# Optimization experiments

Measured on AMD Instinct MI355X. Metric: run time of the kernel, lower is better.

## Reference

```python
import jax, jax.numpy as jnp
import numpy as np

B, S, D_IN, D_EMB, H = 2, 2048, 1024, 1024, 16
HD = D_EMB // H

def setup_inputs() -> dict:
    key = jax.random.key(0)
    k1, k2, k3 = jax.random.split(key, 3)
    # xavier-uniform style scales
    lim_qkv = float(np.sqrt(6.0 / (D_IN + 3 * D_EMB)))
    lim_o = float(np.sqrt(6.0 / (D_EMB + D_EMB)))
    return {
        "x": jax.random.normal(k1, (B, S, D_IN), dtype=jnp.float32),
        "W_qkv": jax.random.uniform(k2, (3 * D_EMB, D_IN), minval=-lim_qkv, maxval=lim_qkv, dtype=jnp.float32),
        "b_qkv": jnp.zeros((3 * D_EMB,), dtype=jnp.float32),
        "W_o": jax.random.uniform(k3, (D_EMB, D_EMB), minval=-lim_o, maxval=lim_o, dtype=jnp.float32),
        "b_o": jnp.zeros((D_EMB,), dtype=jnp.float32),
    }

def reference(x, W_qkv, b_qkv, W_o, b_o):
    b, s, _ = x.shape
    qkv = x @ W_qkv.T + b_qkv                     # [B,S,3E]
    qkv = qkv.reshape(b, s, H, 3 * HD).transpose(0, 2, 1, 3)  # [B,H,S,3*HD]
    q, k, v = jnp.split(qkv, 3, axis=-1)          # each [B,H,S,HD]
    scale = 1.0 / np.sqrt(HD)
    attn = jax.nn.softmax(jnp.einsum('bhqd,bhkd->bhqk', q, k) * scale, axis=-1)
    vals = jnp.einsum('bhqk,bhkd->bhqd', attn, v) # [B,H,S,HD]
    vals = vals.transpose(0, 2, 1, 3).reshape(b, s, D_EMB)
    return vals @ W_o.T + b_o
```

## Files before the change

kernel.cpp:

```cpp
#include <hip/hip_runtime.h>
#include <hip/hip_bf16.h>

typedef unsigned short u16;
typedef unsigned int u32;
typedef __bf16 bf16x8 __attribute__((ext_vector_type(8)));
typedef float f32x4 __attribute__((ext_vector_type(4)));
typedef u32 u32x4 __attribute__((ext_vector_type(4)));

#define MFMA16(a, b, c) __builtin_amdgcn_mfma_f32_16x16x32_bf16((a), (b), (c), 0, 0, 0)

static __device__ __forceinline__ u16 f2bf(float f) {
  __hip_bfloat16 h = __float2bfloat16(f);
  return __builtin_bit_cast(u16, h);
}

static __device__ __forceinline__ u32 pack2(float a, float b) {
  return (u32)f2bf(a) | ((u32)f2bf(b) << 16);
}

static __device__ __forceinline__ bf16x8 ldbf8(const void* p) {
  return *reinterpret_cast<const bf16x8*>(p);
}

static __device__ __forceinline__ void gload_lds16(const void* g, void* l) {
  __builtin_amdgcn_global_load_lds(
      (const __attribute__((address_space(1))) u32*)g,
      (__attribute__((address_space(3))) u32*)l, 16, 0, 0);
}

__global__ void cvt_bf16(const float* __restrict__ s, u16* __restrict__ d, int n8) {
  int i = blockIdx.x * 256 + threadIdx.x;
  if (i >= n8) return;
  const float4* p = reinterpret_cast<const float4*>(s) + (size_t)i * 2;
  float4 a = p[0], b = p[1];
  uint4 o;
  o.x = (u32)f2bf(a.x) | ((u32)f2bf(a.y) << 16);
  o.y = (u32)f2bf(a.z) | ((u32)f2bf(a.w) << 16);
  o.z = (u32)f2bf(b.x) | ((u32)f2bf(b.y) << 16);
  o.w = (u32)f2bf(b.z) | ((u32)f2bf(b.w) << 16);
  reinterpret_cast<uint4*>(d)[i] = o;
}

template <bool BF16OUT>
__global__ __launch_bounds__(256, 3) void gemm_bt(const u16* __restrict__ A,
                                                  const u16* __restrict__ Bm,
                                                  const float* __restrict__ bias,
                                                  void* __restrict__ Cp,
                                                  int M, int N, int K) {
  __shared__ __align__(16) char As[128 * 64 * 2];
  __shared__ __align__(16) char Bs[128 * 64 * 2];
  const int tid = threadIdx.x;
  const int lane = tid & 63;
  const int wid = tid >> 6;
  const int fr = lane & 15, fg = lane >> 4;
  const int gx = gridDim.x, nwg = gx * gridDim.y;
  const int id = blockIdx.y * gx + blockIdx.x;
  const int nid = (id & 7) * (nwg >> 3) + (id >> 3);
  const int bm = nid / gx, bn = nid % gx;
  const int wm = (wid >> 1) * 64, wn = (wid & 1) * 64;

  f32x4 acc[4][4];
#pragma unroll
  for (int i = 0; i < 4; ++i)
#pragma unroll
    for (int j = 0; j < 4; ++j) acc[i][j] = (f32x4){0.f, 0.f, 0.f, 0.f};

  const int nk = K >> 6;
  for (int kt = 0; kt < nk; ++kt) {
#pragma unroll
    for (int it = 0; it < 4; ++it) {
      int q = it * 256 + tid;
      int row = q >> 3;
      int c = (q & 7) ^ (row & 7);
      gload_lds16(A + (size_t)(bm * 128 + row) * K + kt * 64 + c * 8, As + q * 16);
      gload_lds16(Bm + (size_t)(bn * 128 + row) * K + kt * 64 + c * 8, Bs + q * 16);
    }
    __syncthreads();
#pragma unroll
    for (int mk = 0; mk < 2; ++mk) {
      bf16x8 af[4], bfr[4];
#pragma unroll
      for (int i = 0; i < 4; ++i) {
        int row = wm + i * 16 + fr;
        af[i] = ldbf8(As + ((row * 128 + mk * 64 + fg * 16) ^ ((row & 7) << 4)));
      }
#pragma unroll
      for (int j = 0; j < 4; ++j) {
        int row = wn + j * 16 + fr;
        bfr[j] = ldbf8(Bs + ((row * 128 + mk * 64 + fg * 16) ^ ((row & 7) << 4)));
      }
#pragma unroll
      for (int i = 0; i < 4; ++i)
#pragma unroll
        for (int j = 0; j < 4; ++j) acc[i][j] = MFMA16(af[i], bfr[j], acc[i][j]);
    }
    __syncthreads();
  }

#pragma unroll
  for (int j = 0; j < 4; ++j) {
    int col = bn * 128 + wn + j * 16 + fr;
    float bv = bias[col];
#pragma unroll
    for (int i = 0; i < 4; ++i) {
#pragma unroll
      for (int r = 0; r < 4; ++r) {
        int row = bm * 128 + wm + i * 16 + fg * 4 + r;
        float v = acc[i][j][r] + bv;
        if (BF16OUT)
          ((u16*)Cp)[(size_t)row * N + col] = f2bf(v);
        else
          ((float*)Cp)[(size_t)row * N + col] = v;
      }
    }
  }
}

__global__ __launch_bounds__(512, 4) void attn_fwd(const u16* __restrict__ qkv,
                                                   u16* __restrict__ aout) {
  const int qt = blockIdx.x;
  const int bh = blockIdx.y;
  const int b = bh >> 4, h = bh & 15;
  const int tid = threadIdx.x, lane = tid & 63, wid = tid >> 6;
  const int fr = lane & 15, fg = (lane >> 4) & 3;

  __shared__ __align__(16) char Ks[2][64 * 128];
  __shared__ __align__(16) char VTs[2][64 * 128];

  const int q0 = qt * 128 + wid * 16;
  const size_t bS = (size_t)b * 2048;
  const u16* kbase = qkv + bS * 3072 + h * 192 + 64;
  const u16* vbase = qkv + bS * 3072 + h * 192 + 128;

  const int krow = tid >> 3;
  const int kcol = (tid & 7) * 8;
  int kwo = (krow * 128 + (tid & 7) * 16) ^ ((krow & 7) << 4);
  asm volatile("" : "+v"(kwo));
  const int vg = (tid >> 4) & 3;
  const int vs2 = 32 * (wid >> 2) + 16 * (vg >> 1) + 4 * (wid & 3) + 2 * (vg & 1);
  const int vdc = (tid & 15) * 4;
  const int vm_ = vs2 >> 5, vG = (vs2 >> 2) & 3;
  const int vu = ((vs2 >> 4) & 1) * 2 + ((vs2 >> 1) & 1);
  const int vl0 = vm_ * 32 + ((vG ^ vu) << 3) + vu * 2;
  int wof[4];
#pragma unroll
  for (int j = 0; j < 4; ++j) {
    int d = vdc + j;
    wof[j] = ((d * 128 + vl0 * 2) ^ ((((d & 7) ^ ((d >> 3) & 7))) << 4));
    asm volatile("" : "+v"(wof[j]));
  }
  int kro[2];
#pragma unroll
  for (int mk = 0; mk < 2; ++mk) {
    kro[mk] = ((fr * 128 + mk * 64 + fg * 16) ^ ((fr & 7) << 4));
    asm volatile("" : "+v"(kro[mk]));
  }
  int vadr[4][2];
#pragma unroll
  for (int tp = 0; tp < 4; ++tp)
#pragma unroll
    for (int mk = 0; mk < 2; ++mk) {
      int d = tp * 16 + fr;
      int swz = (((d & 7) ^ ((d >> 3) & 7)) << 4);
      vadr[tp][mk] = ((d * 128 + mk * 64 + fg * 16) ^ swz);
      asm volatile("" : "+v"(vadr[tp][mk]));
    }

  bf16x8 qf[2];
#pragma unroll
  for (int mk = 0; mk < 2; ++mk) {
    bf16x8 v = ldbf8(qkv + (bS + q0 + fr) * 3072 + h * 192 + mk * 32 + fg * 8);
#pragma unroll
    for (int e = 0; e < 8; ++e) v[e] = (__bf16)((float)v[e] * 0.1803368801f);
    qf[mk] = v;
  }

  const u32 one2 = 0x3F803F80u;
  const u32x4 onev = {one2, one2, one2, one2};
  const bf16x8 onesf = __builtin_bit_cast(bf16x8, onev);
  float zs = 0.f;
  asm volatile("" : "+v"(zs));
  const f32x4 zacc = {zs, zs, zs, zs};

  f32x4 oacc[4];
#pragma unroll
  for (int t = 0; t < 4; ++t) oacc[t] = (f32x4){0.f, 0.f, 0.f, 0.f};
  f32x4 lacc = (f32x4){0.f, 0.f, 0.f, 0.f};

#define LOADT(S0, KR, V0, V1)                                                  \
  KR = *reinterpret_cast<const uint4*>(kbase + (size_t)((S0) + krow) * 3072 + kcol); \
  V0 = *reinterpret_cast<const uint2*>(vbase + (size_t)((S0) + vs2) * 3072 + vdc);   \
  V1 = *reinterpret_cast<const uint2*>(vbase + (size_t)((S0) + vs2 + 1) * 3072 + vdc);

#define STAGE(BUF, KR, V0, V1)                                      \
  {                                                                 \
    *reinterpret_cast<uint4*>(Ks[BUF] + kwo) = KR;                  \
    const u16* e0 = reinterpret_cast<const u16*>(&V0);              \
    const u16* e1 = reinterpret_cast<const u16*>(&V1);              \
    _Pragma("unroll") for (int j = 0; j < 4; ++j) {                 \
      u32 w = (u32)e0[j] | ((u32)e1[j] << 16);                      \
      *reinterpret_cast<u32*>(VTs[BUF] + wof[j]) = w;               \
    }                                                               \
  }

#define BAR()                                          \
  {                                                    \
    __builtin_amdgcn_sched_barrier(0);                 \
    asm volatile("s_waitcnt lgkmcnt(0)" ::: "memory"); \
    __builtin_amdgcn_s_barrier();                      \
    __builtin_amdgcn_sched_barrier(0);                 \
  }

#define COMPUTE(BUF)                                                           \
  {                                                                            \
    f32x4 sc[4];                                                               \
    __builtin_amdgcn_s_setprio(1);                                             \
    _Pragma("unroll") for (int t = 0; t < 4; ++t) {                            \
      bf16x8 kf0 = ldbf8(Ks[BUF] + kro[0] + t * 2048);                         \
      bf16x8 kf1 = ldbf8(Ks[BUF] + kro[1] + t * 2048);                         \
      sc[t] = MFMA16(kf0, qf[0], zacc);                                        \
      sc[t] = MFMA16(kf1, qf[1], sc[t]);                                       \
    }                                                                          \
    __builtin_amdgcn_s_setprio(0);                                             \
    u32 Wp[2][4];                                                              \
    _Pragma("unroll") for (int t = 0; t < 4; ++t) {                            \
      float p0 = __builtin_amdgcn_exp2f(sc[t][0]);                             \
      float p1 = __builtin_amdgcn_exp2f(sc[t][1]);                             \
      float p2 = __builtin_amdgcn_exp2f(sc[t][2]);                             \
      float p3 = __builtin_amdgcn_exp2f(sc[t][3]);                             \
      Wp[0][t] = pack2(p0, p1);                                                \
      Wp[1][t] = pack2(p2, p3);                                                \
    }                                                                          \
    _Pragma("unroll") for (int mk = 0; mk < 2; ++mk) {                         \
      u32x4 pk;                                                                \
      pk.x = Wp[0][2 * mk];                                                    \
      pk.y = (u32)__shfl_xor((int)Wp[1][2 * mk], 16);                          \
      pk.z = (u32)__shfl_xor((int)Wp[0][2 * mk + 1], 32);                      \
      pk.w = (u32)__shfl_xor((int)Wp[1][2 * mk + 1], 48);                      \
      bf16x8 pa = __builtin_bit_cast(bf16x8, pk);                              \
      __builtin_amdgcn_s_setprio(1);                                           \
      lacc = MFMA16(pa, onesf, lacc);                                          \
      _Pragma("unroll") for (int tp = 0; tp < 4; ++tp) {                       \
        bf16x8 vf = ldbf8(VTs[BUF] + vadr[tp][mk]);                            \
        oacc[tp] = MFMA16(pa, vf, oacc[tp]);                                   \
      }                                                                        \
      __builtin_amdgcn_s_setprio(0);                                           \
    }                                                                          \
  }

  uint4 ka;
  uint2 va0, va1;
  uint4 kb;
  uint2 vb0, vb1;
  LOADT(0, ka, va0, va1);
  for (int kv = 0; kv < 32; kv += 2) {
    LOADT((kv + 1) * 64, kb, vb0, vb1);
    STAGE(0, ka, va0, va1);
    BAR();
    COMPUTE(0);
    {
      int s0n = (kv + 2 < 32) ? (kv + 2) * 64 : 0;
      LOADT(s0n, ka, va0, va1);
    }
    STAGE(1, kb, vb0, vb1);
    BAR();
    COMPUTE(1);
  }
#undef LOADT
#undef STAGE
#undef BAR
#undef COMPUTE

  {
    float invb[4];
#pragma unroll
    for (int r = 0; r < 4; ++r) invb[r] = 1.f / lacc[r];
#pragma unroll
    for (int tp = 0; tp < 4; ++tp) {
#pragma unroll
      for (int r = 0; r < 4; ++r) {
        int row = q0 + fg * 4 + r;
        aout[(bS + row) * 1024 + h * 64 + tp * 16 + fr] =
            f2bf(oacc[tp][r] * invb[r]);
      }
    }
  }
}

extern "C" void kernel_launch(void* const* d_in, const int* in_sizes, int n_in,
                              void* d_out, int out_size, void* d_ws, size_t ws_size,
                              hipStream_t stream) {
  const float* x = (const float*)d_in[0];
  const float* Wqkv = (const float*)d_in[1];
  const float* bqkv = (const float*)d_in[2];
  const float* Wo = (const float*)d_in[3];
  const float* bo = (const float*)d_in[4];
  float* out = (float*)d_out;
  char* ws = (char*)d_ws;

  u16* xb = (u16*)(ws);
  u16* wqb = (u16*)(ws + 8388608);
  u16* wob = (u16*)(ws + 14680064);
  u16* qkvb = (u16*)(ws + 16777216);
  u16* attb = (u16*)(ws + 41943040);

  cvt_bf16<<<2048, 256, 0, stream>>>(x, xb, 524288);
  cvt_bf16<<<1536, 256, 0, stream>>>(Wqkv, wqb, 393216);
  cvt_bf16<<<512, 256, 0, stream>>>(Wo, wob, 131072);

  gemm_bt<true><<<dim3(24, 32), 256, 0, stream>>>(xb, wqb, bqkv, qkvb, 4096, 3072, 1024);
  attn_fwd<<<dim3(16, 32), 512, 0, stream>>>(qkvb, attb);
  gemm_bt<false><<<dim3(8, 32), 256, 0, stream>>>(attb, wob, bo, out, 4096, 1024, 1024);
}
```

Baseline: 117.6 us.

## Process two 16-row query tiles per wave in attention with 256-thread blocks

The attention kernel now uses 4 waves per block instead of 8. Each wave handles 32 query rows as two 16-row tiles, so every K and V fragment read from LDS feeds twice as many MFMAs. Each thread now loads and stages twice as much K/V data per tile, and the launch bounds drop to 256 threads with a minimum of 2 blocks. The aim is less LDS read traffic and fewer waves per block, at the cost of more registers per thread and fewer threads sharing the staging work. The kernel also skips the max-subtraction in softmax, but that was already the case before this change.

```diff
diff --git a/kernel.cpp b/kernel.cpp
--- a/kernel.cpp
+++ b/kernel.cpp
@@ -116,7 +116,7 @@
   }
 }
 
-__global__ __launch_bounds__(512, 4) void attn_fwd(const u16* __restrict__ qkv,
+__global__ __launch_bounds__(256, 2) void attn_fwd(const u16* __restrict__ qkv,
                                                    u16* __restrict__ aout) {
   const int qt = blockIdx.x;
   const int bh = blockIdx.y;
@@ -127,24 +127,24 @@
   __shared__ __align__(16) char Ks[2][64 * 128];
   __shared__ __align__(16) char VTs[2][64 * 128];
 
-  const int q0 = qt * 128 + wid * 16;
+  const int q0 = qt * 128 + wid * 32;
   const size_t bS = (size_t)b * 2048;
   const u16* kbase = qkv + bS * 3072 + h * 192 + 64;
   const u16* vbase = qkv + bS * 3072 + h * 192 + 128;
 
-  const int krow = tid >> 3;
+  const int krow0 = tid >> 3, krow1 = 32 + (tid >> 3);
   const int kcol = (tid & 7) * 8;
-  int kwo = (krow * 128 + (tid & 7) * 16) ^ ((krow & 7) << 4);
-  asm volatile("" : "+v"(kwo));
-  const int vg = (tid >> 4) & 3;
-  const int vs2 = 32 * (wid >> 2) + 16 * (vg >> 1) + 4 * (wid & 3) + 2 * (vg & 1);
-  const int vdc = (tid & 15) * 4;
+  int kw0 = (krow0 * 128 + (tid & 7) * 16) ^ ((krow0 & 7) << 4);
+  int kw1 = (krow1 * 128 + (tid & 7) * 16) ^ ((krow1 & 7) << 4);
+  asm volatile("" : "+v"(kw0), "+v"(kw1));
+  const int vs2 = (tid >> 3) * 2;
+  const int vdc = (tid & 7) * 8;
   const int vm_ = vs2 >> 5, vG = (vs2 >> 2) & 3;
   const int vu = ((vs2 >> 4) & 1) * 2 + ((vs2 >> 1) & 1);
   const int vl0 = vm_ * 32 + ((vG ^ vu) << 3) + vu * 2;
-  int wof[4];
-#pragma unroll
-  for (int j = 0; j < 4; ++j) {
+  int wof[8];
+#pragma unroll
+  for (int j = 0; j < 8; ++j) {
     int d = vdc + j;
     wof[j] = ((d * 128 + vl0 * 2) ^ ((((d & 7) ^ ((d >> 3) & 7))) << 4));
     asm volatile("" : "+v"(wof[j]));
@@ -166,14 +166,17 @@
       asm volatile("" : "+v"(vadr[tp][mk]));
     }
 
-  bf16x8 qf[2];
-#pragma unroll
-  for (int mk = 0; mk < 2; ++mk) {
-    bf16x8 v = ldbf8(qkv + (bS + q0 + fr) * 3072 + h * 192 + mk * 32 + fg * 8);
-#pragma unroll
-    for (int e = 0; e < 8; ++e) v[e] = (__bf16)((float)v[e] * 0.1803368801f);
-    qf[mk] = v;
-  }
+  bf16x8 qf[2][2];
+#pragma unroll
+  for (int qs = 0; qs < 2; ++qs)
+#pragma unroll
+    for (int mk = 0; mk < 2; ++mk) {
+      bf16x8 v =
+          ldbf8(qkv + (bS + q0 + qs * 16 + fr) * 3072 + h * 192 + mk * 32 + fg * 8);
+#pragma unroll
+      for (int e = 0; e < 8; ++e) v[e] = (__bf16)((float)v[e] * 0.1803368801f);
+      qf[qs][mk] = v;
+    }
 
   const u32 one2 = 0x3F803F80u;
   const u32x4 onev = {one2, one2, one2, one2};
@@ -182,25 +185,31 @@
   asm volatile("" : "+v"(zs));
   const f32x4 zacc = {zs, zs, zs, zs};
 
-  f32x4 oacc[4];
-#pragma unroll
-  for (int t = 0; t < 4; ++t) oacc[t] = (f32x4){0.f, 0.f, 0.f, 0.f};
-  f32x4 lacc = (f32x4){0.f, 0.f, 0.f, 0.f};
-
-#define LOADT(S0, KR, V0, V1)                                                  \
-  KR = *reinterpret_cast<const uint4*>(kbase + (size_t)((S0) + krow) * 3072 + kcol); \
-  V0 = *reinterpret_cast<const uint2*>(vbase + (size_t)((S0) + vs2) * 3072 + vdc);   \
-  V1 = *reinterpret_cast<const uint2*>(vbase + (size_t)((S0) + vs2 + 1) * 3072 + vdc);
-
-#define STAGE(BUF, KR, V0, V1)                                      \
-  {                                                                 \
-    *reinterpret_cast<uint4*>(Ks[BUF] + kwo) = KR;                  \
-    const u16* e0 = reinterpret_cast<const u16*>(&V0);              \
-    const u16* e1 = reinterpret_cast<const u16*>(&V1);              \
-    _Pragma("unroll") for (int j = 0; j < 4; ++j) {                 \
-      u32 w = (u32)e0[j] | ((u32)e1[j] << 16);                      \
-      *reinterpret_cast<u32*>(VTs[BUF] + wof[j]) = w;               \
-    }                                                               \
+  f32x4 oacc0[4], oacc1[4];
+#pragma unroll
+  for (int t = 0; t < 4; ++t) {
+    oacc0[t] = (f32x4){0.f, 0.f, 0.f, 0.f};
+    oacc1[t] = (f32x4){0.f, 0.f, 0.f, 0.f};
+  }
+  f32x4 lacc0 = (f32x4){0.f, 0.f, 0.f, 0.f};
+  f32x4 lacc1 = (f32x4){0.f, 0.f, 0.f, 0.f};
+
+#define LOADT(S0, K0, K1, V0, V1)                                                    \
+  K0 = *reinterpret_cast<const uint4*>(kbase + (size_t)((S0) + krow0) * 3072 + kcol); \
+  K1 = *reinterpret_cast<const uint4*>(kbase + (size_t)((S0) + krow1) * 3072 + kcol); \
+  V0 = *reinterpret_cast<const uint4*>(vbase + (size_t)((S0) + vs2) * 3072 + vdc);    \
+  V1 = *reinterpret_cast<const uint4*>(vbase + (size_t)((S0) + vs2 + 1) * 3072 + vdc);
+
+#define STAGE(BUF, K0, K1, V0, V1)                       \
+  {                                                      \
+    *reinterpret_cast<uint4*>(Ks[BUF] + kw0) = K0;       \
+    *reinterpret_cast<uint4*>(Ks[BUF] + kw1) = K1;       \
+    const u16* e0 = reinterpret_cast<const u16*>(&V0);   \
+    const u16* e1 = reinterpret_cast<const u16*>(&V1);   \
+    _Pragma("unroll") for (int j = 0; j < 8; ++j) {      \
+      u32 w = (u32)e0[j] | ((u32)e1[j] << 16);           \
+      *reinterpret_cast<u32*>(VTs[BUF] + wof[j]) = w;    \
+    }                                                    \
   }
 
 #define BAR()                                          \
@@ -213,56 +222,65 @@
 
 #define COMPUTE(BUF)                                                           \
   {                                                                            \
-    f32x4 sc[4];                                                               \
+    f32x4 sc0[4], sc1[4];                                                      \
     __builtin_amdgcn_s_setprio(1);                                             \
     _Pragma("unroll") for (int t = 0; t < 4; ++t) {                            \
       bf16x8 kf0 = ldbf8(Ks[BUF] + kro[0] + t * 2048);                         \
       bf16x8 kf1 = ldbf8(Ks[BUF] + kro[1] + t * 2048);                         \
-      sc[t] = MFMA16(kf0, qf[0], zacc);                                        \
-      sc[t] = MFMA16(kf1, qf[1], sc[t]);                                       \
+      sc0[t] = MFMA16(kf0, qf[0][0], zacc);                                    \
+      sc0[t] = MFMA16(kf1, qf[0][1], sc0[t]);                                  \
+      sc1[t] = MFMA16(kf0, qf[1][0], zacc);                                    \
+      sc1[t] = MFMA16(kf1, qf[1][1], sc1[t]);                                  \
     }                                                                          \
     __builtin_amdgcn_s_setprio(0);                                             \
-    u32 Wp[2][4];                                                              \
+    u32 Wp0[2][4], Wp1[2][4];                                                  \
     _Pragma("unroll") for (int t = 0; t < 4; ++t) {                            \
-      float p0 = __builtin_amdgcn_exp2f(sc[t][0]);                             \
-      float p1 = __builtin_amdgcn_exp2f(sc[t][1]);                             \
-      float p2 = __builtin_amdgcn_exp2f(sc[t][2]);                             \
-      float p3 = __builtin_amdgcn_exp2f(sc[t][3]);                             \
-      Wp[0][t] = pack2(p0, p1);                                                \
-      Wp[1][t] = pack2(p2, p3);                                                \
+      Wp0[0][t] = pack2(__builtin_amdgcn_exp2f(sc0[t][0]),                     \
+                        __builtin_amdgcn_exp2f(sc0[t][1]));                    \
+      Wp0[1][t] = pack2(__builtin_amdgcn_exp2f(sc0[t][2]),                     \
+                        __builtin_amdgcn_exp2f(sc0[t][3]));                    \
+      Wp1[0][t] = pack2(__builtin_amdgcn_exp2f(sc1[t][0]),                     \
+                        __builtin_amdgcn_exp2f(sc1[t][1]));                    \
+      Wp1[1][t] = pack2(__builtin_amdgcn_exp2f(sc1[t][2]),                     \
+                        __builtin_amdgcn_exp2f(sc1[t][3]));                    \
     }                                                                          \
     _Pragma("unroll") for (int mk = 0; mk < 2; ++mk) {                         \
-      u32x4 pk;                                                                \
-      pk.x = Wp[0][2 * mk];                                                    \
-      pk.y = (u32)__shfl_xor((int)Wp[1][2 * mk], 16);                          \
-      pk.z = (u32)__shfl_xor((int)Wp[0][2 * mk + 1], 32);                      \
-      pk.w = (u32)__shfl_xor((int)Wp[1][2 * mk + 1], 48);                      \
-      bf16x8 pa = __builtin_bit_cast(bf16x8, pk);                              \
+      u32x4 pk0, pk1;                                                          \
+      pk0.x = Wp0[0][2 * mk];                                                  \
+      pk0.y = (u32)__shfl_xor((int)Wp0[1][2 * mk], 16);                        \
+      pk0.z = (u32)__shfl_xor((int)Wp0[0][2 * mk + 1], 32);                    \
+      pk0.w = (u32)__shfl_xor((int)Wp0[1][2 * mk + 1], 48);                    \
+      pk1.x = Wp1[0][2 * mk];                                                  \
+      pk1.y = (u32)__shfl_xor((int)Wp1[1][2 * mk], 16);                        \
+      pk1.z = (u32)__shfl_xor((int)Wp1[0][2 * mk + 1], 32);                    \
+      pk1.w = (u32)__shfl_xor((int)Wp1[1][2 * mk + 1], 48);                    \
+      bf16x8 pa0 = __builtin_bit_cast(bf16x8, pk0);                            \
+      bf16x8 pa1 = __builtin_bit_cast(bf16x8, pk1);                            \
       __builtin_amdgcn_s_setprio(1);                                           \
-      lacc = MFMA16(pa, onesf, lacc);                                          \
+      lacc0 = MFMA16(pa0, onesf, lacc0);                                       \
+      lacc1 = MFMA16(pa1, onesf, lacc1);                                       \
       _Pragma("unroll") for (int tp = 0; tp < 4; ++tp) {                       \
         bf16x8 vf = ldbf8(VTs[BUF] + vadr[tp][mk]);                            \
-        oacc[tp] = MFMA16(pa, vf, oacc[tp]);                                   \
+        oacc0[tp] = MFMA16(pa0, vf, oacc0[tp]);                                \
+        oacc1[tp] = MFMA16(pa1, vf, oacc1[tp]);                                \
       }                                                                        \
       __builtin_amdgcn_s_setprio(0);                                           \
     }                                                                          \
   }
 
-  uint4 ka;
-  uint2 va0, va1;
-  uint4 kb;
-  uint2 vb0, vb1;
-  LOADT(0, ka, va0, va1);
+  uint4 ka0, ka1, va0, va1;
+  uint4 kb0, kb1, vb0, vb1;
+  LOADT(0, ka0, ka1, va0, va1);
   for (int kv = 0; kv < 32; kv += 2) {
-    LOADT((kv + 1) * 64, kb, vb0, vb1);
-    STAGE(0, ka, va0, va1);
+    LOADT((kv + 1) * 64, kb0, kb1, vb0, vb1);
+    STAGE(0, ka0, ka1, va0, va1);
     BAR();
     COMPUTE(0);
     {
       int s0n = (kv + 2 < 32) ? (kv + 2) * 64 : 0;
-      LOADT(s0n, ka, va0, va1);
-    }
-    STAGE(1, kb, vb0, vb1);
+      LOADT(s0n, ka0, ka1, va0, va1);
+    }
+    STAGE(1, kb0, kb1, vb0, vb1);
     BAR();
     COMPUTE(1);
   }
@@ -272,16 +290,22 @@
 #undef COMPUTE
 
   {
-    float invb[4];
-#pragma unroll
-    for (int r = 0; r < 4; ++r) invb[r] = 1.f / lacc[r];
+    float invb0[4], invb1[4];
+#pragma unroll
+    for (int r = 0; r < 4; ++r) {
+      invb0[r] = 1.f / lacc0[r];
+      invb1[r] = 1.f / lacc1[r];
+    }
 #pragma unroll
     for (int tp = 0; tp < 4; ++tp) {
 #pragma unroll
       for (int r = 0; r < 4; ++r) {
-        int row = q0 + fg * 4 + r;
-        aout[(bS + row) * 1024 + h * 64 + tp * 16 + fr] =
-            f2bf(oacc[tp][r] * invb[r]);
+        int row0 = q0 + fg * 4 + r;
+        aout[(bS + row0) * 1024 + h * 64 + tp * 16 + fr] =
+            f2bf(oacc0[tp][r] * invb0[r]);
+        int row1 = q0 + 16 + fg * 4 + r;
+        aout[(bS + row1) * 1024 + h * 64 + tp * 16 + fr] =
+            f2bf(oacc1[tp][r] * invb1[r]);
       }
     }
   }
@@ -309,6 +333,6 @@
   cvt_bf16<<<512, 256, 0, stream>>>(Wo, wob, 131072);
 
   gemm_bt<true><<<dim3(24, 32), 256, 0, stream>>>(xb, wqb, bqkv, qkvb, 4096, 3072, 1024);
-  attn_fwd<<<dim3(16, 32), 512, 0, stream>>>(qkvb, attb);
+  attn_fwd<<<dim3(16, 32), 256, 0, stream>>>(qkvb, attb);
   gemm_bt<false><<<dim3(8, 32), 256, 0, stream>>>(attb, wob, bo, out, 4096, 1024, 1024);
 }
```

New measurement: 114.4 us. -2.7%, faster.
